# Kernel optimization log

Hardware: AMD Instinct MI355X
Metric: run time of the kernel (lower is better)

Reference implementation:

```python
import jax, jax.numpy as jnp
import numpy as np

DIM_IN = 512
DIM_K = 64
NUM_HEADS = 32


def setup_inputs() -> dict:
    key = jax.random.key(0)
    ks = jax.random.split(key, 6)
    B, N = 2, 2048
    inner = DIM_K * NUM_HEADS
    s_in = 1.0 / np.sqrt(DIM_IN)
    s_inner = 1.0 / np.sqrt(inner)
    return {
        "x": jax.random.normal(ks[0], (B, N, DIM_IN), dtype=jnp.float32),
        "Wq": jax.random.uniform(ks[1], (DIM_IN, inner), jnp.float32, -s_in, s_in),
        "Wk": jax.random.uniform(ks[2], (DIM_IN, inner), jnp.float32, -s_in, s_in),
        "Wv": jax.random.uniform(ks[3], (DIM_IN, inner), jnp.float32, -s_in, s_in),
        "Wz": jax.random.uniform(ks[4], (inner, DIM_IN), jnp.float32, -s_inner, s_inner),
        "bz": jax.random.uniform(ks[5], (DIM_IN,), jnp.float32, -s_inner, s_inner),
    }


def reference(x, Wq, Wk, Wv, Wz, bz):
    B, N, _ = x.shape
    H, Dk = NUM_HEADS, DIM_K
    scale = 1.0 / np.sqrt(Dk)
    # project then split heads: [B, N, H*Dk] -> [B, H, N, Dk]
    def heads(t):
        return t.reshape(B, N, H, Dk).transpose(0, 2, 1, 3)
    q = heads(x @ Wq)
    k = heads(x @ Wk)
    v = heads(x @ Wv)
    # scores: [B, H, N, N]
    dist = jnp.einsum("bhqd,bhkd->bhqk", q, k) * scale
    dist = jax.nn.softmax(dist, axis=-1)
    att = jnp.einsum("bhqk,bhkd->bhqd", dist, v)  # [B, H, N, Dk]
    att = att.transpose(0, 2, 1, 3).reshape(B, N, H * Dk)
    return att @ Wz + bz
```

## Files before the change

kernel.cpp:

```cpp
#include <hip/hip_runtime.h>

#define HEADS 32
#define DK    64
#define NSEQ  2048
#define BATCH 2
#define DIN   512
#define INNER 2048

typedef float f32x2 __attribute__((ext_vector_type(2)));
typedef float f32x4 __attribute__((ext_vector_type(4)));
typedef float f32x16 __attribute__((ext_vector_type(16)));
typedef short s16x8 __attribute__((ext_vector_type(8)));
typedef short s16x4 __attribute__((ext_vector_type(4)));
typedef unsigned u32x2 __attribute__((ext_vector_type(2)));
typedef unsigned u32x4 __attribute__((ext_vector_type(4)));

#define AS1 __attribute__((address_space(1)))
#define AS3 __attribute__((address_space(3)))

__device__ __forceinline__ short f2b(float f) {
  unsigned u = __float_as_uint(f);
  u += 0x7fffu + ((u >> 16) & 1u);
  return (short)(u >> 16);
}

__device__ __forceinline__ unsigned cvt_pk_bf16(float lo, float hi) {
  unsigned r;
  asm("v_cvt_pk_bf16_f32 %0, %1, %2" : "=v"(r) : "v"(lo), "v"(hi));
  return r;
}

__device__ __forceinline__ float xhalf_add(float v) {
  u32x2 r = __builtin_amdgcn_permlane32_swap(__float_as_uint(v), __float_as_uint(v),
                                             false, false);
  return __uint_as_float(r[0]) + __uint_as_float(r[1]);
}

__device__ __forceinline__ void gll16(const short* gp, short* lp) {
  __builtin_amdgcn_global_load_lds((const AS1 unsigned*)gp, (AS3 unsigned*)lp, 16, 0, 0);
}


__global__ __launch_bounds__(256) void k_cvt(const float* __restrict__ in,
                                             short* __restrict__ out) {
  int t = blockIdx.x * 256 + threadIdx.x;
  int m = t >> 6, kc = t & 63;
  const float* src = in + (size_t)m * 512 + kc * 8;
  float4 v0 = *reinterpret_cast<const float4*>(src);
  float4 v1 = *reinterpret_cast<const float4*>(src + 4);
  s16x8 o;
  o[0] = f2b(v0.x); o[1] = f2b(v0.y); o[2] = f2b(v0.z); o[3] = f2b(v0.w);
  o[4] = f2b(v1.x); o[5] = f2b(v1.y); o[6] = f2b(v1.z); o[7] = f2b(v1.w);
  size_t lin = (size_t)(m >> 4) * 8192 + (kc >> 2) * 512 + (kc & 3) * 128 + (m & 15) * 8;
  *reinterpret_cast<s16x8*>(out + lin) = o;
}

__global__ __launch_bounds__(256) void k_transpose_qkv(const float* __restrict__ Wq,
                                                       const float* __restrict__ Wk,
                                                       const float* __restrict__ Wv,
                                                       short* __restrict__ outb) {
  const float* in = blockIdx.z == 0 ? Wq : blockIdx.z == 1 ? Wk : Wv;
  short* out = outb + (size_t)blockIdx.z * 1048576;
  __shared__ float tile[64][65];
  const int tc = blockIdx.x * 64;
  const int tr = blockIdx.y * 64;
  const int tx = threadIdx.x & 63;
  const int ty = threadIdx.x >> 6;
#pragma unroll
  for (int rr = ty; rr < 64; rr += 4)
    tile[rr][tx] = in[(size_t)(tr + rr) * INNER + tc + tx];
  __syncthreads();
#pragma unroll
  for (int rr = ty; rr < 64; rr += 4) {
    int n = tc + rr, k = tr + tx;
    size_t lin = (size_t)(n >> 4) * (DIN * 16) + (k >> 5) * 512 +
                 ((k >> 3) & 3) * 128 + (n & 15) * 8 + (k & 7);
    out[lin] = f2b(tile[tx][rr]);
  }
}

__global__ __launch_bounds__(256) void k_transpose(const float* __restrict__ in,
                                                   short* __restrict__ out,
                                                   int R, int C) {
  __shared__ float tile[64][65];
  const int tc = blockIdx.x * 64;
  const int tr = blockIdx.y * 64;
  const int tx = threadIdx.x & 63;
  const int ty = threadIdx.x >> 6;
#pragma unroll
  for (int rr = ty; rr < 64; rr += 4)
    tile[rr][tx] = in[(size_t)(tr + rr) * C + tc + tx];
  __syncthreads();
#pragma unroll
  for (int rr = ty; rr < 64; rr += 4) {
    int n = tc + rr, k = tr + tx;
    size_t lin = (size_t)(n >> 4) * ((size_t)R * 16) + (k >> 5) * 512 +
                 ((k >> 3) & 3) * 128 + (n & 15) * 8 + (k & 7);
    out[lin] = f2b(tile[tx][rr]);
  }
}

__global__ __launch_bounds__(256) void k_gemm_qkv(const short* __restrict__ A,
                                                  const short* __restrict__ Bw,
                                                  short* __restrict__ Qb,
                                                  short* __restrict__ Kb,
                                                  short* __restrict__ Vb) {
  __shared__ short sA[2][4096];
  __shared__ short sB[2][4096];
  const int bm = blockIdx.x * 128;
  const int bn = blockIdx.y * 128;
  const int wave = threadIdx.x >> 6, lane = threadIdx.x & 63;
  const int l16 = lane & 15, g = lane >> 4;
  const int wr = wave >> 1, wc = wave & 1;

  const short* Au = A + ((size_t)(bm >> 4) + wave) * 8192 + lane * 8;
  const short* Bu = Bw + ((size_t)(bn >> 4) + wave) * 8192 + lane * 8;

  f32x4 acc[4][4] = {};

  auto stage = [&](int buf, int kt) {
    gll16(Au + kt * 512,              &sA[buf][wave * 512]);
    gll16(Au + 4 * 8192 + kt * 512,   &sA[buf][(wave + 4) * 512]);
    gll16(Bu + kt * 512,              &sB[buf][wave * 512]);
    gll16(Bu + 4 * 8192 + kt * 512,   &sB[buf][(wave + 4) * 512]);
  };

  stage(0, 0);
  __syncthreads();
  int cur = 0;
  for (int kt = 0; kt < 16; ++kt) {
    if (kt + 1 < 16) stage(cur ^ 1, kt + 1);
    s16x8 a[4], b[4];
#pragma unroll
    for (int i = 0; i < 4; i++)
      a[i] = *reinterpret_cast<const s16x8*>(&sA[cur][(wr * 4 + i) * 512 + lane * 8]);
#pragma unroll
    for (int c = 0; c < 4; c++)
      b[c] = *reinterpret_cast<const s16x8*>(&sB[cur][(wc * 4 + c) * 512 + lane * 8]);
#pragma unroll
    for (int i = 0; i < 4; i++)
#pragma unroll
      for (int c = 0; c < 4; c++)
        acc[i][c] = __builtin_amdgcn_mfma_f32_16x16x32_bf16(a[i], b[c], acc[i][c], 0, 0, 0);
    if (kt + 1 < 16) { __syncthreads(); cur ^= 1; }
  }

  const int proj = bn >> 11;
#pragma unroll
  for (int i = 0; i < 4; i++)
#pragma unroll
    for (int c = 0; c < 4; c++) {
      int n0  = bm + wr * 64 + i * 16 + 4 * g;
      int col = bn + wc * 64 + c * 16 + l16;
      int b = n0 >> 11, n = n0 & 2047;
      int nc = col & 2047;
      int h = nc >> 6, dk = nc & 63;
      size_t hb = (size_t)(b * HEADS + h) * (NSEQ * DK);
      if (proj == 2) {
        size_t idx = hb + (size_t)(n >> 5) * 2048 + ((n >> 4) & 1) * 1024 +
                     (dk >> 5) * 512 + ((n >> 3) & 1) * 256 + (dk & 31) * 8 + (n & 7);
        s16x4 w;
#pragma unroll
        for (int r = 0; r < 4; r++) w[r] = f2b(acc[i][c][r]);
        *reinterpret_cast<s16x4*>(Vb + idx) = w;
      } else {
#pragma unroll
        for (int r = 0; r < 4; r++) {
          int nr = n + r;
          size_t idx = hb + (size_t)(nr >> 5) * 2048 + (dk >> 4) * 512 +
                       ((dk >> 3) & 1) * 256 + (nr & 31) * 8 + (dk & 7);
          float v = acc[i][c][r];
          if (proj == 0) Qb[idx] = f2b(v * 0.18033688f);
          else           Kb[idx] = f2b(v);
        }
      }
    }
}

__global__ __launch_bounds__(256) void k_gemm_out(const short* __restrict__ A,
                                                  const short* __restrict__ Bw,
                                                  float* __restrict__ out,
                                                  const float* __restrict__ bias) {
  __shared__ short sA[2][4096];
  __shared__ short sB[2][4096];
  const int bm = blockIdx.x * 64;
  const int bn = blockIdx.y * 64;
  const int wave = threadIdx.x >> 6, lane = threadIdx.x & 63;
  const int l16 = lane & 15, g = lane >> 4;
  const int wr = wave >> 1, wc = wave & 1;

  const short* Au = A + (size_t)(bm >> 4) * 32768 + lane * 8;
  const short* Bu = Bw + (size_t)(bn >> 4) * 32768 + lane * 8;

  f32x4 acc[2][2] = {};

  auto stage = [&](int buf, int kt) {
    gll16(Au + (size_t)wave * 32768 + (2 * kt)     * 512, &sA[buf][(wave * 2 + 0) * 512]);
    gll16(Au + (size_t)wave * 32768 + (2 * kt + 1) * 512, &sA[buf][(wave * 2 + 1) * 512]);
    gll16(Bu + (size_t)wave * 32768 + (2 * kt)     * 512, &sB[buf][(wave * 2 + 0) * 512]);
    gll16(Bu + (size_t)wave * 32768 + (2 * kt + 1) * 512, &sB[buf][(wave * 2 + 1) * 512]);
  };

  stage(0, 0);
  __syncthreads();
  int cur = 0;
  for (int kt = 0; kt < 32; ++kt) {
    if (kt + 1 < 32) stage(cur ^ 1, kt + 1);
#pragma unroll
    for (int ku = 0; ku < 2; ++ku) {
      s16x8 a[2], b[2];
#pragma unroll
      for (int i = 0; i < 2; i++)
        a[i] = *reinterpret_cast<const s16x8*>(
            &sA[cur][((wr * 2 + i) * 2 + ku) * 512 + lane * 8]);
#pragma unroll
      for (int c = 0; c < 2; c++)
        b[c] = *reinterpret_cast<const s16x8*>(
            &sB[cur][((wc * 2 + c) * 2 + ku) * 512 + lane * 8]);
#pragma unroll
      for (int i = 0; i < 2; i++)
#pragma unroll
        for (int c = 0; c < 2; c++)
          acc[i][c] = __builtin_amdgcn_mfma_f32_16x16x32_bf16(a[i], b[c], acc[i][c], 0, 0, 0);
    }
    if (kt + 1 < 32) { __syncthreads(); cur ^= 1; }
  }

#pragma unroll
  for (int i = 0; i < 2; i++)
#pragma unroll
    for (int c = 0; c < 2; c++)
#pragma unroll
      for (int r = 0; r < 4; r++) {
        int row = bm + wr * 32 + i * 16 + 4 * g + r;
        int col = bn + wc * 32 + c * 16 + l16;
        out[(size_t)row * 512 + col] = acc[i][c][r] + bias[col];
      }
}

__global__ __launch_bounds__(128) void k_attn(const short* __restrict__ Q,
                                              const short* __restrict__ K,
                                              const short* __restrict__ VT,
                                              short* __restrict__ att) {
  const int wave = threadIdx.x >> 6, lane = threadIdx.x & 63;
  const int l32 = lane & 31, hi = lane >> 5;
  const int h = blockIdx.y, b = blockIdx.z;
  const int q0 = blockIdx.x * 128 + wave * 64;
  const size_t hb = ((size_t)b * HEADS + h) * (size_t)NSEQ * DK;
  const short* Qh = Q + hb;
  const short* Kh = K + hb;
  const short* Vh = VT + hb;

  s16x8 qfA[4], qfB[4];
  {
    const short* qa = Qh + (size_t)(q0 >> 5) * 2048 + lane * 8;
#pragma unroll
    for (int c = 0; c < 4; c++) qfA[c] = *reinterpret_cast<const s16x8*>(qa + c * 512);
    const short* qb2 = qa + 2048;
#pragma unroll
    for (int c = 0; c < 4; c++) qfB[c] = *reinterpret_cast<const s16x8*>(qb2 + c * 512);
  }

  f32x16 otA[2] = {}, otB[2] = {};
  float lsA = 0.f, lsB = 0.f;

  constexpr int NT = NSEQ / 32;
  s16x8 kfA[4], kfB[4];
  {
    const short* kbase = Kh + lane * 8;
#pragma unroll
    for (int c = 0; c < 4; c++) kfA[c] = *reinterpret_cast<const s16x8*>(kbase + c * 512);
  }

  auto softmax_frag = [&](f32x16& st, float& ls, s16x8& pf0, s16x8& pf1) {
    float p[16];
#pragma unroll
    for (int r = 0; r < 16; r++) p[r] = __builtin_amdgcn_exp2f(st[r]);
    f32x2 e0 = (f32x2){p[0], p[1]} + (f32x2){p[2], p[3]};
    f32x2 e1 = (f32x2){p[4], p[5]} + (f32x2){p[6], p[7]};
    f32x2 e2 = (f32x2){p[8], p[9]} + (f32x2){p[10], p[11]};
    f32x2 e3 = (f32x2){p[12], p[13]} + (f32x2){p[14], p[15]};
    e0 += e1; e2 += e3; e0 += e2;
    ls += xhalf_add(e0[0] + e0[1]);
    unsigned a0 = cvt_pk_bf16(p[0], p[1]),   a1 = cvt_pk_bf16(p[2], p[3]);
    unsigned a2 = cvt_pk_bf16(p[4], p[5]),   a3 = cvt_pk_bf16(p[6], p[7]);
    unsigned a4 = cvt_pk_bf16(p[8], p[9]),   a5 = cvt_pk_bf16(p[10], p[11]);
    unsigned a6 = cvt_pk_bf16(p[12], p[13]), a7 = cvt_pk_bf16(p[14], p[15]);
    u32x2 w0 = __builtin_amdgcn_permlane32_swap(a0, a2, false, false);
    u32x2 w1 = __builtin_amdgcn_permlane32_swap(a1, a3, false, false);
    u32x2 w2 = __builtin_amdgcn_permlane32_swap(a4, a6, false, false);
    u32x2 w3 = __builtin_amdgcn_permlane32_swap(a5, a7, false, false);
    u32x4 pw0 = {w0[0], w1[0], w0[1], w1[1]};
    u32x4 pw1 = {w2[0], w3[0], w2[1], w3[1]};
    pf0 = __builtin_bit_cast(s16x8, pw0);
    pf1 = __builtin_bit_cast(s16x8, pw1);
  };

  auto body = [&](s16x8(&kc)[4], s16x8(&kn)[4], int t) {
    const short* vbase = Vh + (size_t)t * 2048 + lane * 8;
    s16x8 vf00 = *reinterpret_cast<const s16x8*>(vbase);
    s16x8 vf01 = *reinterpret_cast<const s16x8*>(vbase + 512);
    s16x8 vf10 = *reinterpret_cast<const s16x8*>(vbase + 1024);
    s16x8 vf11 = *reinterpret_cast<const s16x8*>(vbase + 1536);

    int tn = (t + 1 < NT) ? t + 1 : t;
    const short* kbase = Kh + (size_t)tn * 2048 + lane * 8;
#pragma unroll
    for (int c = 0; c < 4; c++) kn[c] = *reinterpret_cast<const s16x8*>(kbase + c * 512);

    f32x16 stA = {}, stB = {};
#pragma unroll
    for (int c = 0; c < 4; c++)
      stA = __builtin_amdgcn_mfma_f32_32x32x16_bf16(kc[c], qfA[c], stA, 0, 0, 0);
#pragma unroll
    for (int c = 0; c < 4; c++)
      stB = __builtin_amdgcn_mfma_f32_32x32x16_bf16(kc[c], qfB[c], stB, 0, 0, 0);

    s16x8 pA0, pA1, pB0, pB1;
    softmax_frag(stA, lsA, pA0, pA1);
    softmax_frag(stB, lsB, pB0, pB1);

    otA[0] = __builtin_amdgcn_mfma_f32_32x32x16_bf16(vf00, pA0, otA[0], 0, 0, 0);
    otA[1] = __builtin_amdgcn_mfma_f32_32x32x16_bf16(vf01, pA0, otA[1], 0, 0, 0);
    otB[0] = __builtin_amdgcn_mfma_f32_32x32x16_bf16(vf00, pB0, otB[0], 0, 0, 0);
    otB[1] = __builtin_amdgcn_mfma_f32_32x32x16_bf16(vf01, pB0, otB[1], 0, 0, 0);
    otA[0] = __builtin_amdgcn_mfma_f32_32x32x16_bf16(vf10, pA1, otA[0], 0, 0, 0);
    otA[1] = __builtin_amdgcn_mfma_f32_32x32x16_bf16(vf11, pA1, otA[1], 0, 0, 0);
    otB[0] = __builtin_amdgcn_mfma_f32_32x32x16_bf16(vf10, pB1, otB[0], 0, 0, 0);
    otB[1] = __builtin_amdgcn_mfma_f32_32x32x16_bf16(vf11, pB1, otB[1], 0, 0, 0);
  };

  for (int t = 0; t < NT; t += 2) {
    body(kfA, kfB, t);
    body(kfB, kfA, t + 1);
  }

  auto wout = [&](f32x16(&ot)[2], float ls, int qq) {
    float inv = 1.f / ls;
    size_t aunit = ((size_t)(b * 128) + (size_t)((qq + l32) >> 4)) * 32768;
    const int mr = l32 & 15;
#pragma unroll
    for (int dt = 0; dt < 2; dt++)
#pragma unroll
      for (int gq = 0; gq < 4; gq++) {
        s16x4 w;
#pragma unroll
        for (int j = 0; j < 4; j++) w[j] = f2b(ot[dt][4 * gq + j] * inv);
        size_t base = aunit + (size_t)(h * 2 + dt) * 512 + gq * 128 + mr * 8 + 4 * hi;
        *reinterpret_cast<s16x4*>(att + base) = w;
      }
  };
  wout(otA, lsA, q0);
  wout(otB, lsB, q0 + 32);
}

extern "C" void kernel_launch(void* const* d_in, const int* in_sizes, int n_in,
                              void* d_out, int out_size, void* d_ws, size_t ws_size,
                              hipStream_t stream) {
  const float* x  = (const float*)d_in[0];
  const float* Wq = (const float*)d_in[1];
  const float* Wk = (const float*)d_in[2];
  const float* Wv = (const float*)d_in[3];
  const float* Wz = (const float*)d_in[4];
  const float* bz = (const float*)d_in[5];

  char* ws = (char*)d_ws;
  const size_t MB = (size_t)1 << 20;
  short* xb   = (short*)(ws);
  short* wqkv = (short*)(ws + 4 * MB);
  short* wzt  = (short*)(ws + 10 * MB);
  short* Qb   = (short*)(ws + 12 * MB);
  short* Kb   = (short*)(ws + 28 * MB);
  short* Vt   = (short*)(ws + 44 * MB);
  short* att  = (short*)(ws + 60 * MB);

  k_cvt<<<1024, 256, 0, stream>>>(x, xb);
  k_transpose_qkv<<<dim3(32, 8, 3), 256, 0, stream>>>(Wq, Wk, Wv, wqkv);
  k_transpose<<<dim3(8, 32), 256, 0, stream>>>(Wz, wzt, INNER, DIN);

  k_gemm_qkv<<<dim3(32, 48), 256, 0, stream>>>(xb, wqkv, Qb, Kb, Vt);

  k_attn<<<dim3(NSEQ / 128, HEADS, BATCH), 128, 0, stream>>>(Qb, Kb, Vt, att);

  k_gemm_out<<<dim3(64, 8), 256, 0, stream>>>(att, wzt, (float*)d_out, bz);
}
```

Measured before the change: 166.8 us.

## Merge prep kernels into one launch and remap attention blocks per XCD

Folds the three preprocessing kernels (x conversion, QKV weight transpose, Wz transpose) into a single k_prep launch that picks its work by block index. It also flattens the attention grid to 1D and remaps block ids so all 16 query tiles of a (batch, head) pair land on the same XCD, letting them share K/V through that XCD's L2. The goals are to cut launch overhead and to raise L2 hit rates for K/V. The risk is that k_prep now reserves shared memory for every block, including the conversion blocks that never use it.

```diff
diff --git a/kernel.cpp b/kernel.cpp
--- a/kernel.cpp
+++ b/kernel.cpp
@@ -41,50 +41,42 @@
 }
 
 
-__global__ __launch_bounds__(256) void k_cvt(const float* __restrict__ in,
-                                             short* __restrict__ out) {
-  int t = blockIdx.x * 256 + threadIdx.x;
-  int m = t >> 6, kc = t & 63;
-  const float* src = in + (size_t)m * 512 + kc * 8;
-  float4 v0 = *reinterpret_cast<const float4*>(src);
-  float4 v1 = *reinterpret_cast<const float4*>(src + 4);
-  s16x8 o;
-  o[0] = f2b(v0.x); o[1] = f2b(v0.y); o[2] = f2b(v0.z); o[3] = f2b(v0.w);
-  o[4] = f2b(v1.x); o[5] = f2b(v1.y); o[6] = f2b(v1.z); o[7] = f2b(v1.w);
-  size_t lin = (size_t)(m >> 4) * 8192 + (kc >> 2) * 512 + (kc & 3) * 128 + (m & 15) * 8;
-  *reinterpret_cast<s16x8*>(out + lin) = o;
-}
-
-__global__ __launch_bounds__(256) void k_transpose_qkv(const float* __restrict__ Wq,
-                                                       const float* __restrict__ Wk,
-                                                       const float* __restrict__ Wv,
-                                                       short* __restrict__ outb) {
-  const float* in = blockIdx.z == 0 ? Wq : blockIdx.z == 1 ? Wk : Wv;
-  short* out = outb + (size_t)blockIdx.z * 1048576;
+__global__ __launch_bounds__(256) void k_prep(const float* __restrict__ x,
+                                              const float* __restrict__ Wq,
+                                              const float* __restrict__ Wk,
+                                              const float* __restrict__ Wv,
+                                              const float* __restrict__ Wz,
+                                              short* __restrict__ xb,
+                                              short* __restrict__ wqkv,
+                                              short* __restrict__ wzt) {
+  const int bid = blockIdx.x;
+  if (bid < 1024) {
+    int t = bid * 256 + threadIdx.x;
+    int m = t >> 6, kc = t & 63;
+    const float* src = x + (size_t)m * 512 + kc * 8;
+    float4 v0 = *reinterpret_cast<const float4*>(src);
+    float4 v1 = *reinterpret_cast<const float4*>(src + 4);
+    s16x8 o;
+    o[0] = f2b(v0.x); o[1] = f2b(v0.y); o[2] = f2b(v0.z); o[3] = f2b(v0.w);
+    o[4] = f2b(v1.x); o[5] = f2b(v1.y); o[6] = f2b(v1.z); o[7] = f2b(v1.w);
+    size_t lin = (size_t)(m >> 4) * 8192 + (kc >> 2) * 512 + (kc & 3) * 128 + (m & 15) * 8;
+    *reinterpret_cast<s16x8*>(xb + lin) = o;
+    return;
+  }
   __shared__ float tile[64][65];
-  const int tc = blockIdx.x * 64;
-  const int tr = blockIdx.y * 64;
-  const int tx = threadIdx.x & 63;
-  const int ty = threadIdx.x >> 6;
-#pragma unroll
-  for (int rr = ty; rr < 64; rr += 4)
-    tile[rr][tx] = in[(size_t)(tr + rr) * INNER + tc + tx];
-  __syncthreads();
-#pragma unroll
-  for (int rr = ty; rr < 64; rr += 4) {
-    int n = tc + rr, k = tr + tx;
-    size_t lin = (size_t)(n >> 4) * (DIN * 16) + (k >> 5) * 512 +
-                 ((k >> 3) & 3) * 128 + (n & 15) * 8 + (k & 7);
-    out[lin] = f2b(tile[tx][rr]);
-  }
-}
-
-__global__ __launch_bounds__(256) void k_transpose(const float* __restrict__ in,
-                                                   short* __restrict__ out,
-                                                   int R, int C) {
-  __shared__ float tile[64][65];
-  const int tc = blockIdx.x * 64;
-  const int tr = blockIdx.y * 64;
+  const float* in; short* out; int R, C, bx, by;
+  if (bid < 1792) {
+    int z = (bid - 1024) >> 8, inner = (bid - 1024) & 255;
+    in = z == 0 ? Wq : z == 1 ? Wk : Wv;
+    out = wqkv + (size_t)z * 1048576;
+    R = DIN; C = INNER;
+    bx = inner & 31; by = inner >> 5;
+  } else {
+    int inner = bid - 1792;
+    in = Wz; out = wzt; R = INNER; C = DIN;
+    bx = inner & 7; by = inner >> 3;
+  }
+  const int tc = bx * 64, tr = by * 64;
   const int tx = threadIdx.x & 63;
   const int ty = threadIdx.x >> 6;
 #pragma unroll
@@ -244,8 +236,12 @@
                                               short* __restrict__ att) {
   const int wave = threadIdx.x >> 6, lane = threadIdx.x & 63;
   const int l32 = lane & 31, hi = lane >> 5;
-  const int h = blockIdx.y, b = blockIdx.z;
-  const int q0 = blockIdx.x * 128 + wave * 64;
+  const int bid = blockIdx.x;
+  const int xcd = bid & 7, slot = bid >> 3;
+  const int g = xcd * 8 + (slot >> 4);
+  const int qt = slot & 15;
+  const int h = g & 31, b = g >> 5;
+  const int q0 = qt * 128 + wave * 64;
   const size_t hb = ((size_t)b * HEADS + h) * (size_t)NSEQ * DK;
   const short* Qh = Q + hb;
   const short* Kh = K + hb;
@@ -374,13 +370,11 @@
   short* Vt   = (short*)(ws + 44 * MB);
   short* att  = (short*)(ws + 60 * MB);
 
-  k_cvt<<<1024, 256, 0, stream>>>(x, xb);
-  k_transpose_qkv<<<dim3(32, 8, 3), 256, 0, stream>>>(Wq, Wk, Wv, wqkv);
-  k_transpose<<<dim3(8, 32), 256, 0, stream>>>(Wz, wzt, INNER, DIN);
+  k_prep<<<2048, 256, 0, stream>>>(x, Wq, Wk, Wv, Wz, xb, wqkv, wzt);
 
   k_gemm_qkv<<<dim3(32, 48), 256, 0, stream>>>(xb, wqkv, Qb, Kb, Vt);
 
-  k_attn<<<dim3(NSEQ / 128, HEADS, BATCH), 128, 0, stream>>>(Qb, Kb, Vt, att);
+  k_attn<<<1024, 128, 0, stream>>>(Qb, Kb, Vt, att);
 
   k_gemm_out<<<dim3(64, 8), 256, 0, stream>>>(att, wzt, (float*)d_out, bz);
 }
```

Measured after the change: 152.1 us (median of 2 runs). 8.8% less time.
